# Optimization experiments

Measured on AMD Instinct MI355X. Metric: run time of the kernel, lower is better.

The kernel has to match this reference:

```python
import jax, jax.numpy as jnp
import numpy as np

STD = 0.5
B = 1048576
DIM = 8  # arch == 2
_LOG_STD = -0.6931471805599453       # log(0.5)
_HALF_LOG_2PI = 0.9189385332046727   # 0.5*log(2*pi)


def _mlp(x, w1, b1, w2, b2):
    # Sequential(Linear, ReLU, Linear)
    return jnp.maximum(x @ w1 + b1, 0.0) @ w2 + b2


def _bce_sum(logits, targets):
    # BCEWithLogitsLoss(reduction='sum'), numerically stable
    return jnp.sum(jnp.maximum(logits, 0.0) - logits * targets
                   + jnp.log1p(jnp.exp(-jnp.abs(logits))))


def _normal_logprob_sum(mu, y):
    # D.Normal(mu, STD).log_prob(y).sum()
    return jnp.sum(-0.5 * ((y - mu) / STD) ** 2 - _LOG_STD - _HALF_LOG_2PI)


def setup_inputs() -> dict:
    key = jax.random.key(0)
    keys = iter(jax.random.split(key, 64))

    def nrm(shape, s=1.0):
        return s * jax.random.normal(next(keys), shape, dtype=jnp.float32)

    inp = {
        'y1': nrm((B, 1)),
        'y2': nrm((B, 1)),
        'n1': jax.random.uniform(next(keys), (B, 2), dtype=jnp.float32),
        'n2': jax.random.uniform(next(keys), (B, 2), dtype=jnp.float32),
        'n3': jax.random.uniform(next(keys), (B, 2), dtype=jnp.float32),
        'n4': jax.random.uniform(next(keys), (B, 2), dtype=jnp.float32),
    }
    # (name, d_in, d_out) for every 2-layer MLP in infnet/gennet
    mlp_specs = [('inf0', 2, 2), ('inf1', 3, 2), ('inf2', 1, 2), ('inf3', 2, 2),
                 ('g1', 2, 2), ('g2', 2, 1), ('g3', 1, 2), ('g4', 2, 2), ('g5', 2, 1)]
    for name, din, dout in mlp_specs:
        inp[name + '_w1'] = nrm((din, DIM), 0.5)
        inp[name + '_b1'] = nrm((DIM,), 0.1)
        inp[name + '_w2'] = nrm((DIM, dout), 0.5)
        inp[name + '_b2'] = nrm((dout,), 0.1)
    inp['g0_w'] = nrm((1, 2), 0.5)  # gennet[0]: Linear(1, z, bias=False)
    return inp


def reference(y1, y2, n1, n2, n3, n4,
              inf0_w1, inf0_b1, inf0_w2, inf0_b2,
              inf1_w1, inf1_b1, inf1_w2, inf1_b2,
              inf2_w1, inf2_b1, inf2_w2, inf2_b2,
              inf3_w1, inf3_b1, inf3_w2, inf3_b2,
              g1_w1, g1_b1, g1_w2, g1_b2,
              g2_w1, g2_b1, g2_w2, g2_b2,
              g3_w1, g3_b1, g3_w2, g3_b2,
              g4_w1, g4_b1, g4_w2, g4_b2,
              g5_w1, g5_b1, g5_w2, g5_b2,
              g0_w):
    b = y1.shape[0]
    # ---- infer(): recognition pass with hard Bernoulli samples ----
    pz1 = jax.nn.sigmoid(_mlp(jnp.concatenate([y1, y2], axis=1),
                              inf0_w1, inf0_b1, inf0_w2, inf0_b2))
    z1 = (pz1 > n1).astype(jnp.float32)
    pz2 = jax.nn.sigmoid(_mlp(jnp.concatenate([y2, z1], axis=1),
                              inf1_w1, inf1_b1, inf1_w2, inf1_b2))
    z2 = (pz2 > n2).astype(jnp.float32)
    pz3 = jax.nn.sigmoid(_mlp(y2, inf2_w1, inf2_b1, inf2_w2, inf2_b2))
    z3 = (pz3 > n3).astype(jnp.float32)
    pz4 = jax.nn.sigmoid(_mlp(z3, inf3_w1, inf3_b1, inf3_w2, inf3_b2))
    z4 = (pz4 > n4).astype(jnp.float32)
    # ---- generate_wake(): generative logits conditioned on inferred latents ----
    l4 = jnp.ones((b, 1), jnp.float32) @ g0_w          # [B, 2]
    l3 = _mlp(z4, g1_w1, g1_b1, g1_w2, g1_b2)          # [B, 2]
    muy2 = _mlp(z3, g2_w1, g2_b1, g2_w2, g2_b2)        # [B, 1]
    l2 = _mlp(y2, g3_w1, g3_b1, g3_w2, g3_b2)          # [B, 2]
    l1 = _mlp(z2, g4_w1, g4_b1, g4_w2, g4_b2)          # [B, 2]
    muy1 = _mlp(z1, g5_w1, g5_b1, g5_w2, g5_b2)        # [B, 1]
    # ---- wake losses ----
    bf = jnp.float32(b)
    loss_z = (_bce_sum(l1, z1) + _bce_sum(l2, z2)
              + _bce_sum(l3, z3) + _bce_sum(l4, z4)) / bf
    loss_y = (-_normal_logprob_sum(muy1, y1)
              - _normal_logprob_sum(muy2, y2)) / bf
    return (loss_z + loss_y, loss_z, loss_y)
```

## Files before the change

kernel.cpp:

```cpp
#include <hip/hip_runtime.h>

#define NB 1024
#define NT 256

__device__ __forceinline__ float bce_f(float l, float t) {
    float e = __expf(-fabsf(l));
    return fmaxf(l, 0.0f) - l * t + __logf(1.0f + e);
}

__device__ __forceinline__ float z_from(float s, float n) {
    float e = __expf(-s);
    return (1.0f - n > n * e) ? 1.0f : 0.0f;
}

__global__ __launch_bounds__(NT) void wake_main(
    const float* __restrict__ y1, const float* __restrict__ y2,
    const float* __restrict__ n1, const float* __restrict__ n2,
    const float* __restrict__ n3, const float* __restrict__ n4,
    const float* __restrict__ i0w1, const float* __restrict__ i0b1,
    const float* __restrict__ i0w2, const float* __restrict__ i0b2,
    const float* __restrict__ i1w1, const float* __restrict__ i1b1,
    const float* __restrict__ i1w2, const float* __restrict__ i1b2,
    const float* __restrict__ i2w1, const float* __restrict__ i2b1,
    const float* __restrict__ i2w2, const float* __restrict__ i2b2,
    const float* __restrict__ i3w1, const float* __restrict__ i3b1,
    const float* __restrict__ i3w2, const float* __restrict__ i3b2,
    const float* __restrict__ g1w1, const float* __restrict__ g1b1,
    const float* __restrict__ g1w2, const float* __restrict__ g1b2,
    const float* __restrict__ g2w1, const float* __restrict__ g2b1,
    const float* __restrict__ g2w2, const float* __restrict__ g2b2,
    const float* __restrict__ g3w1, const float* __restrict__ g3b1,
    const float* __restrict__ g3w2, const float* __restrict__ g3b2,
    const float* __restrict__ g4w1, const float* __restrict__ g4b1,
    const float* __restrict__ g4w2, const float* __restrict__ g4b2,
    const float* __restrict__ g5w1, const float* __restrict__ g5b1,
    const float* __restrict__ g5w2, const float* __restrict__ g5b2,
    const float* __restrict__ g0w,
    float2* __restrict__ partials)
{
    __shared__ float lds_eval[5][4][2];
    __shared__ float lds_coef[40];

    const int tid = threadIdx.x;
    const int g = blockIdx.x * NT + tid;

    const float4 vy1  = reinterpret_cast<const float4*>(y1)[g];
    const float4 vy2  = reinterpret_cast<const float4*>(y2)[g];
    const float4 n1lo = reinterpret_cast<const float4*>(n1)[2*g];
    const float4 n1hi = reinterpret_cast<const float4*>(n1)[2*g+1];
    const float4 n2lo = reinterpret_cast<const float4*>(n2)[2*g];
    const float4 n2hi = reinterpret_cast<const float4*>(n2)[2*g+1];
    const float4 n3lo = reinterpret_cast<const float4*>(n3)[2*g];
    const float4 n3hi = reinterpret_cast<const float4*>(n3)[2*g+1];
    const float4 n4lo = reinterpret_cast<const float4*>(n4)[2*g];
    const float4 n4hi = reinterpret_cast<const float4*>(n4)[2*g+1];

    if (tid < 20) {
        const int m = tid >> 2, c = tid & 3;
        const float z0 = (float)(c & 1), z1f = (float)(c >> 1);
        const float *w1, *bb1, *w2, *bb2; int dout;
        switch (m) {
            case 0:  w1 = i3w1; bb1 = i3b1; w2 = i3w2; bb2 = i3b2; dout = 2; break;
            case 1:  w1 = g1w1; bb1 = g1b1; w2 = g1w2; bb2 = g1b2; dout = 2; break;
            case 2:  w1 = g2w1; bb1 = g2b1; w2 = g2w2; bb2 = g2b2; dout = 1; break;
            case 3:  w1 = g4w1; bb1 = g4b1; w2 = g4w2; bb2 = g4b2; dout = 2; break;
            default: w1 = g5w1; bb1 = g5b1; w2 = g5w2; bb2 = g5b2; dout = 1; break;
        }
        float o0 = bb2[0];
        float o1 = (dout == 2) ? bb2[1] : 0.0f;
        #pragma unroll
        for (int j = 0; j < 8; ++j) {
            float h = fmaxf(bb1[j] + z0 * w1[j] + z1f * w1[8 + j], 0.0f);
            o0 += h * w2[j * dout];
            if (dout == 2) o1 += h * w2[j * 2 + 1];
        }
        lds_eval[m][c][0] = o0;
        lds_eval[m][c][1] = o1;
    }
    __syncthreads();
    if (tid < 10) {
        const int m = tid >> 1, k = tid & 1;
        const float f00 = lds_eval[m][0][k], f10 = lds_eval[m][1][k];
        const float f01 = lds_eval[m][2][k], f11 = lds_eval[m][3][k];
        lds_coef[tid * 4 + 0] = f00;
        lds_coef[tid * 4 + 1] = f10 - f00;
        lds_coef[tid * 4 + 2] = f01 - f00;
        lds_coef[tid * 4 + 3] = f11 - f10 - f01 + f00;
    }
    __syncthreads();

    const float l40 = g0w[0], l41 = g0w[1];

    const float Y1a[4] = {vy1.x, vy1.y, vy1.z, vy1.w};
    const float Y2a[4] = {vy2.x, vy2.y, vy2.z, vy2.w};
    const float N1a[8] = {n1lo.x, n1lo.y, n1lo.z, n1lo.w, n1hi.x, n1hi.y, n1hi.z, n1hi.w};
    const float N2a[8] = {n2lo.x, n2lo.y, n2lo.z, n2lo.w, n2hi.x, n2hi.y, n2hi.z, n2hi.w};
    const float N3a[8] = {n3lo.x, n3lo.y, n3lo.z, n3lo.w, n3hi.x, n3hi.y, n3hi.z, n3hi.w};
    const float N4a[8] = {n4lo.x, n4lo.y, n4lo.z, n4lo.w, n4hi.x, n4hi.y, n4hi.z, n4hi.w};

    float lz = 0.0f, ly = 0.0f;
    #pragma unroll
    for (int s = 0; s < 4; ++s) {
        const float Y1 = Y1a[s], Y2 = Y2a[s];
        float s10 = i0b2[0], s11 = i0b2[1];
        #pragma unroll
        for (int j = 0; j < 8; ++j) {
            float h = fmaxf(i0b1[j] + Y1 * i0w1[j] + Y2 * i0w1[8 + j], 0.0f);
            s10 += h * i0w2[2 * j]; s11 += h * i0w2[2 * j + 1];
        }
        const float z10 = z_from(s10, N1a[2 * s]);
        const float z11 = z_from(s11, N1a[2 * s + 1]);
        float s20 = i1b2[0], s21 = i1b2[1];
        #pragma unroll
        for (int j = 0; j < 8; ++j) {
            float h = fmaxf(i1b1[j] + Y2 * i1w1[j] + z10 * i1w1[8 + j] + z11 * i1w1[16 + j], 0.0f);
            s20 += h * i1w2[2 * j]; s21 += h * i1w2[2 * j + 1];
        }
        const float z20 = z_from(s20, N2a[2 * s]);
        const float z21 = z_from(s21, N2a[2 * s + 1]);
        float s30 = i2b2[0], s31 = i2b2[1];
        #pragma unroll
        for (int j = 0; j < 8; ++j) {
            float h = fmaxf(i2b1[j] + Y2 * i2w1[j], 0.0f);
            s30 += h * i2w2[2 * j]; s31 += h * i2w2[2 * j + 1];
        }
        const float z30 = z_from(s30, N3a[2 * s]);
        const float z31 = z_from(s31, N3a[2 * s + 1]);
        const float p3 = z30 * z31;
        const float s40 = lds_coef[0] + lds_coef[1] * z30 + lds_coef[2] * z31 + lds_coef[3] * p3;
        const float s41 = lds_coef[4] + lds_coef[5] * z30 + lds_coef[6] * z31 + lds_coef[7] * p3;
        const float z40 = z_from(s40, N4a[2 * s]);
        const float z41 = z_from(s41, N4a[2 * s + 1]);
        const float p4 = z40 * z41;
        const float l30 = lds_coef[8]  + lds_coef[9]  * z40 + lds_coef[10] * z41 + lds_coef[11] * p4;
        const float l31 = lds_coef[12] + lds_coef[13] * z40 + lds_coef[14] * z41 + lds_coef[15] * p4;
        const float muy2 = lds_coef[16] + lds_coef[17] * z30 + lds_coef[18] * z31 + lds_coef[19] * p3;
        float l20 = g3b2[0], l21 = g3b2[1];
        #pragma unroll
        for (int j = 0; j < 8; ++j) {
            float h = fmaxf(g3b1[j] + Y2 * g3w1[j], 0.0f);
            l20 += h * g3w2[2 * j]; l21 += h * g3w2[2 * j + 1];
        }
        const float p2 = z20 * z21;
        const float l10 = lds_coef[24] + lds_coef[25] * z20 + lds_coef[26] * z21 + lds_coef[27] * p2;
        const float l11 = lds_coef[28] + lds_coef[29] * z20 + lds_coef[30] * z21 + lds_coef[31] * p2;
        const float p1 = z10 * z11;
        const float muy1 = lds_coef[32] + lds_coef[33] * z10 + lds_coef[34] * z11 + lds_coef[35] * p1;

        lz += bce_f(l10, z10) + bce_f(l11, z11)
            + bce_f(l20, z20) + bce_f(l21, z21)
            + bce_f(l30, z30) + bce_f(l31, z31)
            - l40 * z40 - l41 * z41;
        const float d1 = Y1 - muy1, d2 = Y2 - muy2;
        ly += 2.0f * (d1 * d1) + 2.0f * (d2 * d2);
    }

    #pragma unroll
    for (int off = 32; off > 0; off >>= 1) {
        lz += __shfl_down(lz, off);
        ly += __shfl_down(ly, off);
    }
    __shared__ float2 wsum[NT / 64];
    const int lane = tid & 63, wid = tid >> 6;
    if (lane == 0) wsum[wid] = make_float2(lz, ly);
    __syncthreads();
    if (tid == 0) {
        float a = 0.0f, b = 0.0f;
        #pragma unroll
        for (int w = 0; w < NT / 64; ++w) { a += wsum[w].x; b += wsum[w].y; }
        partials[blockIdx.x] = make_float2(a, b);
    }
}

__global__ __launch_bounds__(256) void wake_reduce(
    const float2* __restrict__ partials, const float* __restrict__ g0w,
    float* __restrict__ out)
{
    const int tid = threadIdx.x;
    float lz = 0.0f, ly = 0.0f;
    #pragma unroll
    for (int i = 0; i < NB / 256; ++i) {
        float2 p = partials[tid + i * 256];
        lz += p.x; ly += p.y;
    }
    #pragma unroll
    for (int off = 32; off > 0; off >>= 1) {
        lz += __shfl_down(lz, off);
        ly += __shfl_down(ly, off);
    }
    __shared__ float2 wsum[4];
    const int lane = tid & 63, wid = tid >> 6;
    if (lane == 0) wsum[wid] = make_float2(lz, ly);
    __syncthreads();
    if (tid == 0) {
        float a = 0.0f, b = 0.0f;
        #pragma unroll
        for (int w = 0; w < 4; ++w) { a += wsum[w].x; b += wsum[w].y; }
        const float l40 = g0w[0], l41 = g0w[1];
        const float C4 = fmaxf(l40, 0.0f) + __logf(1.0f + __expf(-fabsf(l40)))
                       + fmaxf(l41, 0.0f) + __logf(1.0f + __expf(-fabsf(l41)));
        const float inv = 1.0f / 1048576.0f;
        const float loss_z = a * inv + C4;
        const float loss_y = b * inv + 0.4515827052894548f;
        out[0] = loss_z + loss_y;
        out[1] = loss_z;
        out[2] = loss_y;
    }
}

extern "C" void kernel_launch(void* const* d_in, const int* in_sizes, int n_in,
                              void* d_out, int out_size, void* d_ws, size_t ws_size,
                              hipStream_t stream) {
    const float* p[43];
    for (int i = 0; i < 43; ++i) p[i] = (const float*)d_in[i];
    float2* partials = (float2*)d_ws;
    wake_main<<<NB, NT, 0, stream>>>(
        p[0], p[1], p[2], p[3], p[4], p[5],
        p[6], p[7], p[8], p[9],
        p[10], p[11], p[12], p[13],
        p[14], p[15], p[16], p[17],
        p[18], p[19], p[20], p[21],
        p[22], p[23], p[24], p[25],
        p[26], p[27], p[28], p[29],
        p[30], p[31], p[32], p[33],
        p[34], p[35], p[36], p[37],
        p[38], p[39], p[40], p[41],
        p[42], partials);
    wake_reduce<<<1, 256, 0, stream>>>(partials, p[42], (float*)d_out);
}
```

Measured before the change: 26.56 us.

## Precompute bilinear tables in separate kernel, one sample per thread, table-driven softplus

Moves the per-block evaluation of the binary-input MLPs into a separate one-block kernel that writes bilinear coefficient tables to workspace. The tables also cover the sigmoid for z4 and the softplus terms of the l1/l3 BCE, so the main kernel skips those transcendentals. The main kernel changes from four samples per thread with float4 loads to one sample per thread over four times as many blocks, dropping the per-block LDS setup and two barriers. The cost is an extra kernel launch, narrower loads and a larger partials array to reduce.

```diff
diff --git a/kernel.cpp b/kernel.cpp
--- a/kernel.cpp
+++ b/kernel.cpp
@@ -1,60 +1,33 @@
 #include <hip/hip_runtime.h>
-
-#define NB 1024
+#include <math.h>
+
+#define NBLK 4096
 #define NT 256
-
-__device__ __forceinline__ float bce_f(float l, float t) {
-    float e = __expf(-fabsf(l));
-    return fmaxf(l, 0.0f) - l * t + __logf(1.0f + e);
-}
-
-__device__ __forceinline__ float z_from(float s, float n) {
+#define TBL_OFF (NBLK * 8)
+
+__device__ __forceinline__ float zsel(float s, float n) {
     float e = __expf(-s);
     return (1.0f - n > n * e) ? 1.0f : 0.0f;
 }
-
-__global__ __launch_bounds__(NT) void wake_main(
-    const float* __restrict__ y1, const float* __restrict__ y2,
-    const float* __restrict__ n1, const float* __restrict__ n2,
-    const float* __restrict__ n3, const float* __restrict__ n4,
-    const float* __restrict__ i0w1, const float* __restrict__ i0b1,
-    const float* __restrict__ i0w2, const float* __restrict__ i0b2,
-    const float* __restrict__ i1w1, const float* __restrict__ i1b1,
-    const float* __restrict__ i1w2, const float* __restrict__ i1b2,
-    const float* __restrict__ i2w1, const float* __restrict__ i2b1,
-    const float* __restrict__ i2w2, const float* __restrict__ i2b2,
+__device__ __forceinline__ float sp_f(float l) {
+    return fmaxf(l, 0.0f) + __logf(1.0f + __expf(-fabsf(l)));
+}
+
+__global__ __launch_bounds__(64) void make_tables(
     const float* __restrict__ i3w1, const float* __restrict__ i3b1,
     const float* __restrict__ i3w2, const float* __restrict__ i3b2,
     const float* __restrict__ g1w1, const float* __restrict__ g1b1,
     const float* __restrict__ g1w2, const float* __restrict__ g1b2,
     const float* __restrict__ g2w1, const float* __restrict__ g2b1,
     const float* __restrict__ g2w2, const float* __restrict__ g2b2,
-    const float* __restrict__ g3w1, const float* __restrict__ g3b1,
-    const float* __restrict__ g3w2, const float* __restrict__ g3b2,
     const float* __restrict__ g4w1, const float* __restrict__ g4b1,
     const float* __restrict__ g4w2, const float* __restrict__ g4b2,
     const float* __restrict__ g5w1, const float* __restrict__ g5b1,
     const float* __restrict__ g5w2, const float* __restrict__ g5b2,
-    const float* __restrict__ g0w,
-    float2* __restrict__ partials)
+    float* __restrict__ tbl)
 {
     __shared__ float lds_eval[5][4][2];
-    __shared__ float lds_coef[40];
-
     const int tid = threadIdx.x;
-    const int g = blockIdx.x * NT + tid;
-
-    const float4 vy1  = reinterpret_cast<const float4*>(y1)[g];
-    const float4 vy2  = reinterpret_cast<const float4*>(y2)[g];
-    const float4 n1lo = reinterpret_cast<const float4*>(n1)[2*g];
-    const float4 n1hi = reinterpret_cast<const float4*>(n1)[2*g+1];
-    const float4 n2lo = reinterpret_cast<const float4*>(n2)[2*g];
-    const float4 n2hi = reinterpret_cast<const float4*>(n2)[2*g+1];
-    const float4 n3lo = reinterpret_cast<const float4*>(n3)[2*g];
-    const float4 n3hi = reinterpret_cast<const float4*>(n3)[2*g+1];
-    const float4 n4lo = reinterpret_cast<const float4*>(n4)[2*g];
-    const float4 n4hi = reinterpret_cast<const float4*>(n4)[2*g+1];
-
     if (tid < 20) {
         const int m = tid >> 2, c = tid & 3;
         const float z0 = (float)(c & 1), z1f = (float)(c >> 1);
@@ -78,82 +51,126 @@
         lds_eval[m][c][1] = o1;
     }
     __syncthreads();
-    if (tid < 10) {
-        const int m = tid >> 1, k = tid & 1;
-        const float f00 = lds_eval[m][0][k], f10 = lds_eval[m][1][k];
-        const float f01 = lds_eval[m][2][k], f11 = lds_eval[m][3][k];
-        lds_coef[tid * 4 + 0] = f00;
-        lds_coef[tid * 4 + 1] = f10 - f00;
-        lds_coef[tid * 4 + 2] = f01 - f00;
-        lds_coef[tid * 4 + 3] = f11 - f10 - f01 + f00;
-    }
-    __syncthreads();
-
-    const float l40 = g0w[0], l41 = g0w[1];
-
-    const float Y1a[4] = {vy1.x, vy1.y, vy1.z, vy1.w};
-    const float Y2a[4] = {vy2.x, vy2.y, vy2.z, vy2.w};
-    const float N1a[8] = {n1lo.x, n1lo.y, n1lo.z, n1lo.w, n1hi.x, n1hi.y, n1hi.z, n1hi.w};
-    const float N2a[8] = {n2lo.x, n2lo.y, n2lo.z, n2lo.w, n2hi.x, n2hi.y, n2hi.z, n2hi.w};
-    const float N3a[8] = {n3lo.x, n3lo.y, n3lo.z, n3lo.w, n3hi.x, n3hi.y, n3hi.z, n3hi.w};
-    const float N4a[8] = {n4lo.x, n4lo.y, n4lo.z, n4lo.w, n4hi.x, n4hi.y, n4hi.z, n4hi.w};
-
-    float lz = 0.0f, ly = 0.0f;
-    #pragma unroll
-    for (int s = 0; s < 4; ++s) {
-        const float Y1 = Y1a[s], Y2 = Y2a[s];
-        float s10 = i0b2[0], s11 = i0b2[1];
-        #pragma unroll
-        for (int j = 0; j < 8; ++j) {
-            float h = fmaxf(i0b1[j] + Y1 * i0w1[j] + Y2 * i0w1[8 + j], 0.0f);
-            s10 += h * i0w2[2 * j]; s11 += h * i0w2[2 * j + 1];
-        }
-        const float z10 = z_from(s10, N1a[2 * s]);
-        const float z11 = z_from(s11, N1a[2 * s + 1]);
-        float s20 = i1b2[0], s21 = i1b2[1];
-        #pragma unroll
-        for (int j = 0; j < 8; ++j) {
-            float h = fmaxf(i1b1[j] + Y2 * i1w1[j] + z10 * i1w1[8 + j] + z11 * i1w1[16 + j], 0.0f);
-            s20 += h * i1w2[2 * j]; s21 += h * i1w2[2 * j + 1];
-        }
-        const float z20 = z_from(s20, N2a[2 * s]);
-        const float z21 = z_from(s21, N2a[2 * s + 1]);
-        float s30 = i2b2[0], s31 = i2b2[1];
-        #pragma unroll
-        for (int j = 0; j < 8; ++j) {
-            float h = fmaxf(i2b1[j] + Y2 * i2w1[j], 0.0f);
-            s30 += h * i2w2[2 * j]; s31 += h * i2w2[2 * j + 1];
-        }
-        const float z30 = z_from(s30, N3a[2 * s]);
-        const float z31 = z_from(s31, N3a[2 * s + 1]);
-        const float p3 = z30 * z31;
-        const float s40 = lds_coef[0] + lds_coef[1] * z30 + lds_coef[2] * z31 + lds_coef[3] * p3;
-        const float s41 = lds_coef[4] + lds_coef[5] * z30 + lds_coef[6] * z31 + lds_coef[7] * p3;
-        const float z40 = z_from(s40, N4a[2 * s]);
-        const float z41 = z_from(s41, N4a[2 * s + 1]);
-        const float p4 = z40 * z41;
-        const float l30 = lds_coef[8]  + lds_coef[9]  * z40 + lds_coef[10] * z41 + lds_coef[11] * p4;
-        const float l31 = lds_coef[12] + lds_coef[13] * z40 + lds_coef[14] * z41 + lds_coef[15] * p4;
-        const float muy2 = lds_coef[16] + lds_coef[17] * z30 + lds_coef[18] * z31 + lds_coef[19] * p3;
-        float l20 = g3b2[0], l21 = g3b2[1];
-        #pragma unroll
-        for (int j = 0; j < 8; ++j) {
-            float h = fmaxf(g3b1[j] + Y2 * g3w1[j], 0.0f);
-            l20 += h * g3w2[2 * j]; l21 += h * g3w2[2 * j + 1];
-        }
-        const float p2 = z20 * z21;
-        const float l10 = lds_coef[24] + lds_coef[25] * z20 + lds_coef[26] * z21 + lds_coef[27] * p2;
-        const float l11 = lds_coef[28] + lds_coef[29] * z20 + lds_coef[30] * z21 + lds_coef[31] * p2;
-        const float p1 = z10 * z11;
-        const float muy1 = lds_coef[32] + lds_coef[33] * z10 + lds_coef[34] * z11 + lds_coef[35] * p1;
-
-        lz += bce_f(l10, z10) + bce_f(l11, z11)
-            + bce_f(l20, z20) + bce_f(l21, z21)
-            + bce_f(l30, z30) + bce_f(l31, z31)
-            - l40 * z40 - l41 * z41;
-        const float d1 = Y1 - muy1, d2 = Y2 - muy2;
-        ly += 2.0f * (d1 * d1) + 2.0f * (d2 * d2);
-    }
+    if (tid < 12) {
+        const int pair = tid >> 1, elem = tid & 1;
+        int m, k, tf;
+        switch (tid) {
+            case 0:  m = 0; k = 0; tf = 1; break;
+            case 1:  m = 0; k = 1; tf = 1; break;
+            case 2:  m = 1; k = 0; tf = 0; break;
+            case 3:  m = 1; k = 1; tf = 0; break;
+            case 4:  m = 1; k = 0; tf = 2; break;
+            case 5:  m = 1; k = 1; tf = 2; break;
+            case 6:  m = 3; k = 0; tf = 0; break;
+            case 7:  m = 3; k = 1; tf = 0; break;
+            case 8:  m = 3; k = 0; tf = 2; break;
+            case 9:  m = 3; k = 1; tf = 2; break;
+            case 10: m = 2; k = 0; tf = 0; break;
+            default: m = 4; k = 0; tf = 0; break;
+        }
+        float f[4];
+        #pragma unroll
+        for (int c = 0; c < 4; ++c) {
+            float x = lds_eval[m][c][k];
+            if (tf == 1)      x = 1.0f / (1.0f + expf(-x));
+            else if (tf == 2) x = fmaxf(x, 0.0f) + log1pf(expf(-fabsf(x)));
+            f[c] = x;
+        }
+        tbl[(pair * 4 + 0) * 2 + elem] = f[0];
+        tbl[(pair * 4 + 1) * 2 + elem] = f[1] - f[0];
+        tbl[(pair * 4 + 2) * 2 + elem] = f[2] - f[0];
+        tbl[(pair * 4 + 3) * 2 + elem] = f[3] - f[1] - f[2] + f[0];
+    }
+}
+
+__global__ __launch_bounds__(NT, 6) void wake_main(
+    const float* __restrict__ y1, const float* __restrict__ y2,
+    const float* __restrict__ n1, const float* __restrict__ n2,
+    const float* __restrict__ n3, const float* __restrict__ n4,
+    const float* __restrict__ i0w1, const float* __restrict__ i0b1,
+    const float* __restrict__ i0w2, const float* __restrict__ i0b2,
+    const float* __restrict__ i1w1, const float* __restrict__ i1b1,
+    const float* __restrict__ i1w2, const float* __restrict__ i1b2,
+    const float* __restrict__ i2w1, const float* __restrict__ i2b1,
+    const float* __restrict__ i2w2, const float* __restrict__ i2b2,
+    const float* __restrict__ g3w1, const float* __restrict__ g3b1,
+    const float* __restrict__ g3w2, const float* __restrict__ g3b2,
+    const float* __restrict__ g0w,
+    const float* __restrict__ tbl,
+    float2* __restrict__ partials)
+{
+    const int tid = threadIdx.x;
+    const int g = blockIdx.x * NT + tid;
+
+    const float Y1 = y1[g];
+    const float Y2 = y2[g];
+    const float2 N1 = reinterpret_cast<const float2*>(n1)[g];
+    const float2 N2 = reinterpret_cast<const float2*>(n2)[g];
+    const float2 N3 = reinterpret_cast<const float2*>(n3)[g];
+    const float2 N4 = reinterpret_cast<const float2*>(n4)[g];
+
+    float a0 = i0b2[0], a1 = i0b2[1];
+    #pragma unroll
+    for (int j = 0; j < 8; ++j) {
+        float h = fmaxf(i0b1[j] + Y1 * i0w1[j] + Y2 * i0w1[8 + j], 0.0f);
+        a0 += h * i0w2[2 * j]; a1 += h * i0w2[2 * j + 1];
+    }
+    const float z10 = zsel(a0, N1.x);
+    const float z11 = zsel(a1, N1.y);
+
+    float b0 = i1b2[0], b1v = i1b2[1];
+    #pragma unroll
+    for (int j = 0; j < 8; ++j) {
+        float h = fmaxf(i1b1[j] + Y2 * i1w1[j] + z10 * i1w1[8 + j]
+                        + z11 * i1w1[16 + j], 0.0f);
+        b0 += h * i1w2[2 * j]; b1v += h * i1w2[2 * j + 1];
+    }
+    const float z20 = zsel(b0, N2.x);
+    const float z21 = zsel(b1v, N2.y);
+
+    float c0 = i2b2[0], c1 = i2b2[1];
+    #pragma unroll
+    for (int j = 0; j < 8; ++j) {
+        float h = fmaxf(i2b1[j] + Y2 * i2w1[j], 0.0f);
+        c0 += h * i2w2[2 * j]; c1 += h * i2w2[2 * j + 1];
+    }
+    const float z30 = zsel(c0, N3.x);
+    const float z31 = zsel(c1, N3.y);
+
+    const float p3 = z30 * z31;
+    const float sg0 = tbl[0] + tbl[2] * z30 + tbl[4] * z31 + tbl[6] * p3;
+    const float sg1 = tbl[1] + tbl[3] * z30 + tbl[5] * z31 + tbl[7] * p3;
+    const float z40 = (sg0 > N4.x) ? 1.0f : 0.0f;
+    const float z41 = (sg1 > N4.y) ? 1.0f : 0.0f;
+    const float p4 = z40 * z41;
+
+    float l20 = g3b2[0], l21 = g3b2[1];
+    #pragma unroll
+    for (int j = 0; j < 8; ++j) {
+        float h = fmaxf(g3b1[j] + Y2 * g3w1[j], 0.0f);
+        l20 += h * g3w2[2 * j]; l21 += h * g3w2[2 * j + 1];
+    }
+
+    const float l3a  = tbl[8]  + tbl[10] * z40 + tbl[12] * z41 + tbl[14] * p4;
+    const float l3b  = tbl[9]  + tbl[11] * z40 + tbl[13] * z41 + tbl[15] * p4;
+    const float SP3a = tbl[16] + tbl[18] * z40 + tbl[20] * z41 + tbl[22] * p4;
+    const float SP3b = tbl[17] + tbl[19] * z40 + tbl[21] * z41 + tbl[23] * p4;
+    const float p2 = z20 * z21;
+    const float l1a  = tbl[24] + tbl[26] * z20 + tbl[28] * z21 + tbl[30] * p2;
+    const float l1b  = tbl[25] + tbl[27] * z20 + tbl[29] * z21 + tbl[31] * p2;
+    const float SP1a = tbl[32] + tbl[34] * z20 + tbl[36] * z21 + tbl[38] * p2;
+    const float SP1b = tbl[33] + tbl[35] * z20 + tbl[37] * z21 + tbl[39] * p2;
+    const float mu2  = tbl[40] + tbl[42] * z30 + tbl[44] * z31 + tbl[46] * p3;
+    const float p1 = z10 * z11;
+    const float mu1  = tbl[41] + tbl[43] * z10 + tbl[45] * z11 + tbl[47] * p1;
+    const float L40 = g0w[0], L41 = g0w[1];
+
+    float lz = (SP1a - l1a * z10) + (SP1b - l1b * z11)
+             + (sp_f(l20) - l20 * z20) + (sp_f(l21) - l21 * z21)
+             + (SP3a - l3a * z30) + (SP3b - l3b * z31)
+             - (L40 * z40 + L41 * z41);
+    const float d1 = Y1 - mu1, d2 = Y2 - mu2;
+    float ly = d1 * d1 + d2 * d2;
 
     #pragma unroll
     for (int off = 32; off > 0; off >>= 1) {
@@ -179,7 +196,7 @@
     const int tid = threadIdx.x;
     float lz = 0.0f, ly = 0.0f;
     #pragma unroll
-    for (int i = 0; i < NB / 256; ++i) {
+    for (int i = 0; i < NBLK / 256; ++i) {
         float2 p = partials[tid + i * 256];
         lz += p.x; ly += p.y;
     }
@@ -197,11 +214,11 @@
         #pragma unroll
         for (int w = 0; w < 4; ++w) { a += wsum[w].x; b += wsum[w].y; }
         const float l40 = g0w[0], l41 = g0w[1];
-        const float C4 = fmaxf(l40, 0.0f) + __logf(1.0f + __expf(-fabsf(l40)))
-                       + fmaxf(l41, 0.0f) + __logf(1.0f + __expf(-fabsf(l41)));
+        const float c4 = fmaxf(l40, 0.0f) + log1pf(expf(-fabsf(l40)))
+                       + fmaxf(l41, 0.0f) + log1pf(expf(-fabsf(l41)));
         const float inv = 1.0f / 1048576.0f;
-        const float loss_z = a * inv + C4;
-        const float loss_y = b * inv + 0.4515827052894548f;
+        const float loss_z = a * inv + c4;
+        const float loss_y = 2.0f * b * inv + 0.4515827052894548f;
         out[0] = loss_z + loss_y;
         out[1] = loss_z;
         out[2] = loss_y;
@@ -214,17 +231,21 @@
     const float* p[43];
     for (int i = 0; i < 43; ++i) p[i] = (const float*)d_in[i];
     float2* partials = (float2*)d_ws;
-    wake_main<<<NB, NT, 0, stream>>>(
+    float* tbl = (float*)((char*)d_ws + TBL_OFF);
+
+    make_tables<<<1, 64, 0, stream>>>(
+        p[18], p[19], p[20], p[21],
+        p[22], p[23], p[24], p[25],
+        p[26], p[27], p[28], p[29],
+        p[34], p[35], p[36], p[37],
+        p[38], p[39], p[40], p[41],
+        tbl);
+    wake_main<<<NBLK, NT, 0, stream>>>(
         p[0], p[1], p[2], p[3], p[4], p[5],
         p[6], p[7], p[8], p[9],
         p[10], p[11], p[12], p[13],
         p[14], p[15], p[16], p[17],
-        p[18], p[19], p[20], p[21],
-        p[22], p[23], p[24], p[25],
-        p[26], p[27], p[28], p[29],
         p[30], p[31], p[32], p[33],
-        p[34], p[35], p[36], p[37],
-        p[38], p[39], p[40], p[41],
-        p[42], partials);
+        p[42], tbl, partials);
     wake_reduce<<<1, 256, 0, stream>>>(partials, p[42], (float*)d_out);
 }
```

After: 25.57 us. -3.7%, faster.
